# Kernel tuning notes

Measured on AMD Instinct MI355X. Metric: run time of the kernel, lower is better.

Reference implementation:

```python
import jax, jax.numpy as jnp
import numpy as np

N = 8192
D = 256

def setup_inputs() -> dict:
    key = jax.random.key(0)
    k1, k2, k3 = jax.random.split(key, 3)
    x = jax.random.normal(k1, (N, D), dtype=jnp.float32)
    adj_matrix = jax.random.uniform(k2, (N, N), dtype=jnp.float32)
    weight = jax.random.normal(k3, (D, D), dtype=jnp.float32) * 0.02
    bias = jnp.zeros((D,), dtype=jnp.float32)
    return {"x": x, "adj_matrix": adj_matrix, "weight": weight, "bias": bias}

def reference(x, adj_matrix, weight, bias):
    # degree = row sums of adjacency
    degree = jnp.sum(adj_matrix, axis=1)  # [N]
    inv_deg = 1.0 / degree               # inverse of diagonal degree matrix
    # D^-1 @ A @ D^-1 == A scaled by inv_deg on rows and columns
    normalized_adj = adj_matrix * inv_deg[:, None] * inv_deg[None, :]  # [N,N]
    h = jnp.matmul(normalized_adj, x)          # [N,D] aggregation
    h = jnp.matmul(h, weight) + bias           # [N,D] transform
    return jax.nn.relu(h)
```

## Files before the change

### kernel.cpp

```cpp
#include <hip/hip_runtime.h>
#include <stdint.h>
#include <stdio.h>

#define NROWS 8192
#define DDIM 256

typedef __attribute__((ext_vector_type(8))) __bf16 bf16x8;
typedef __attribute__((ext_vector_type(4))) float f32x4;
typedef __attribute__((address_space(3))) uint32_t as3u32;
typedef __attribute__((address_space(1))) uint32_t as1u32;

__device__ __forceinline__ void glds16(const void* g, void* l) {
  __builtin_amdgcn_global_load_lds((const as1u32*)g, (as3u32*)l, 16, 0, 0);
}

__device__ __forceinline__ ushort f2b(float f) {
  uint32_t u = __float_as_uint(f);
  return (ushort)((u + 0x7FFFu + ((u >> 16) & 1u)) >> 16);
}

__global__ __launch_bounds__(256) void degree_cast_kernel(const float* __restrict__ A,
                                                          ushort* __restrict__ Ab,
                                                          float* __restrict__ inv_deg) {
  const int row = blockIdx.x * 4 + (threadIdx.x >> 6);
  const int lane = threadIdx.x & 63;
  const float4* r4 = (const float4*)(A + (size_t)row * NROWS);
  ushort* wr = Ab + (size_t)row * NROWS;
  float s = 0.f;
#pragma unroll
  for (int i = 0; i < 32; ++i) {
    float4 v = r4[lane + (i << 6)];
    s += (v.x + v.y) + (v.z + v.w);
    ushort4 b;
    b.x = f2b(v.x); b.y = f2b(v.y); b.z = f2b(v.z); b.w = f2b(v.w);
    *(ushort4*)(wr + (size_t)(lane + (i << 6)) * 4) = b;
  }
#pragma unroll
  for (int o = 32; o > 0; o >>= 1) s += __shfl_xor(s, o, 64);
  if (lane == 0) inv_deg[row] = 1.0f / s;
}

__global__ __launch_bounds__(256) void transpose_scale_kernel(const float* __restrict__ src,
                                                              const float* __restrict__ scale,
                                                              ushort* __restrict__ dst, int K) {
  __shared__ ushort tile[64 * 256];
  const int k0 = blockIdx.x * 64;
  const int w = threadIdx.x >> 6;
  const int lane = threadIdx.x & 63;
#pragma unroll
  for (int i = 0; i < 16; ++i) {
    const int r = w * 16 + i;
    float4 v = *(const float4*)(src + (size_t)(k0 + r) * DDIM + lane * 4);
    const float sc = scale ? scale[k0 + r] : 1.0f;
    ushort4 b;
    b.x = f2b(v.x * sc); b.y = f2b(v.y * sc);
    b.z = f2b(v.z * sc); b.w = f2b(v.w * sc);
    *(ushort4*)&tile[r * 256 + lane * 4] = b;
  }
  __syncthreads();
  const int c = threadIdx.x;
  ushort* drow = dst + (size_t)c * K + k0;
#pragma unroll
  for (int s = 0; s < 8; ++s) {
    uint32_t p[4];
#pragma unroll
    for (int j = 0; j < 4; ++j) {
      uint32_t lo = tile[(s * 8 + 2 * j + 0) * 256 + c];
      uint32_t hi = tile[(s * 8 + 2 * j + 1) * 256 + c];
      p[j] = lo | (hi << 16);
    }
    uint4 u; u.x = p[0]; u.y = p[1]; u.z = p[2]; u.w = p[3];
    *(uint4*)(drow + s * 8) = u;
  }
}

__global__ __launch_bounds__(256, 2) void gemm_big_kernel(
    const ushort* __restrict__ Ab,
    const ushort* __restrict__ Bt,
    const float* __restrict__ rowscale,
    float* __restrict__ Cpart) {
  __shared__ ushort Asm[2][64 * 64];
  __shared__ ushort Bsm[2][256 * 64];

  const int tid = threadIdx.x;
  const int lane = tid & 63;
  const int w = tid >> 6;

  const int ks = blockIdx.x & 3;
  const int mb = blockIdx.x >> 2;
  const int m0 = mb * 64;
  const size_t kstart = (size_t)ks * 2048;

  const int al_r = lane >> 3;
  const int al_c = lane & 7;
  const int asw = al_c ^ al_r;
  const char* agA = (const char*)(Ab + (size_t)(m0 + 16 * w + al_r) * NROWS + kstart) + asw * 16;
  const char* bgB = (const char*)(Bt + (size_t)(64 * w + al_r) * NROWS + kstart) + asw * 16;
  const size_t grp = (size_t)8 * NROWS * 2;

  const int fr = lane & 15;
  const int q = lane >> 4;
  const int fsw = fr & 7;

  f32x4 acc[4][4] = {};
  const int NT = 2048 / 64;

  auto stage = [&](int buf, int t) {
    const size_t koff = (size_t)t * 128;
    glds16(agA + koff, &Asm[buf][(16 * w + 0) * 64]);
    glds16(agA + grp + koff, &Asm[buf][(16 * w + 8) * 64]);
#pragma unroll
    for (int j = 0; j < 8; ++j)
      glds16(bgB + (size_t)j * grp + koff, &Bsm[buf][(64 * w + 8 * j) * 64]);
  };

  stage(0, 0);
  int cur = 0;
  for (int t = 0; t < NT; ++t) {
    __syncthreads();
    if (t + 1 < NT) stage(cur ^ 1, t + 1);
#pragma unroll
    for (int kk = 0; kk < 2; ++kk) {
      uint4 af[4], bfr[4];
#pragma unroll
      for (int m = 0; m < 4; ++m)
        af[m] = *(const uint4*)((const char*)&Asm[cur][0] +
                 ((16 * m + fr) * 128 + (((4 * kk + q) ^ fsw) << 4)));
#pragma unroll
      for (int n = 0; n < 4; ++n)
        bfr[n] = *(const uint4*)((const char*)&Bsm[cur][0] +
                 ((64 * w + 16 * n + fr) * 128 + (((4 * kk + q) ^ fsw) << 4)));
#pragma unroll
      for (int m = 0; m < 4; ++m)
#pragma unroll
        for (int n = 0; n < 4; ++n)
          acc[m][n] = __builtin_amdgcn_mfma_f32_16x16x32_bf16(
              __builtin_bit_cast(bf16x8, af[m]), __builtin_bit_cast(bf16x8, bfr[n]),
              acc[m][n], 0, 0, 0);
    }
    cur ^= 1;
  }

  float* Cp = Cpart + (size_t)ks * ((size_t)NROWS * DDIM);
#pragma unroll
  for (int m = 0; m < 4; ++m)
#pragma unroll
    for (int r = 0; r < 4; ++r) {
      const int row = m0 + 16 * m + q * 4 + r;
      const float sc = rowscale[row];
#pragma unroll
      for (int n = 0; n < 4; ++n) {
        const int col = 64 * w + 16 * n + fr;
        Cp[(size_t)row * DDIM + col] = acc[m][n][r] * sc;
      }
    }
}

__global__ __launch_bounds__(512, 4) void gemm_small_kernel(
    const float* __restrict__ Hp,
    const ushort* __restrict__ Bt,
    const float* __restrict__ bias, float* __restrict__ C) {
  const int K = DDIM;
  const size_t PS = (size_t)NROWS * DDIM;
  __shared__ ushort Asm[2][32 * 32];
  __shared__ ushort Bsm[2][256 * 32];

  const int tid = threadIdx.x;
  const int lane = tid & 63;
  const int w = tid >> 6;
  const int m0 = blockIdx.x * 32;

  f32x4 acc[2][2] = {};
  const int NT = K >> 5;

  const int arow = tid >> 3;
  const int aseg = tid & 7;
  const float* ag = Hp + (size_t)(m0 + arow) * DDIM + aseg * 4;
  const int awoff = arow * 32 + ((((aseg >> 1) ^ ((arow >> 1) & 3)) << 3) | ((aseg & 1) << 2));

  const int bch0 = w * 2;
  const int bq = lane >> 2;
  const int bswz = (lane & 3) ^ ((lane >> 3) & 3);
  const char* bg0 = (const char*)Bt + (size_t)(bch0 * 16 + bq) * ((size_t)K * 2) + bswz * 16;
  const char* bg1 = bg0 + (size_t)16 * ((size_t)K * 2);

  const int fr = lane & 15;
  const int fsw = (fr >> 1) & 3;
  const int fch = (lane >> 4) ^ fsw;
  const int aoff0 = fr * 32 + (fch << 3);
  const int aoff1 = (16 + fr) * 32 + (fch << 3);
  const int boff0 = (w * 32 + fr) * 32 + (fch << 3);
  const int boff1 = (w * 32 + 16 + fr) * 32 + (fch << 3);

  auto loadA = [&](int t) {
    float4 u0 = *(const float4*)(ag + 0 * PS + t * 32);
    float4 u1 = *(const float4*)(ag + 1 * PS + t * 32);
    float4 u2 = *(const float4*)(ag + 2 * PS + t * 32);
    float4 u3 = *(const float4*)(ag + 3 * PS + t * 32);
    float4 v;
    v.x = (u0.x + u1.x) + (u2.x + u3.x);
    v.y = (u0.y + u1.y) + (u2.y + u3.y);
    v.z = (u0.z + u1.z) + (u2.z + u3.z);
    v.w = (u0.w + u1.w) + (u2.w + u3.w);
    return v;
  };

  if (tid < 256) {
    float4 v = loadA(0);
    ushort4 b; b.x = f2b(v.x); b.y = f2b(v.y); b.z = f2b(v.z); b.w = f2b(v.w);
    *(ushort4*)&Asm[0][awoff] = b;
  }
  glds16(bg0, &Bsm[0][(bch0 + 0) * 512]);
  glds16(bg1, &Bsm[0][(bch0 + 1) * 512]);

  int cur = 0;
  for (int t = 0; t < NT; ++t) {
    __syncthreads();
    const bool pf = (t + 1 < NT);
    float4 av;
    if (pf) {
      if (tid < 256) av = loadA(t + 1);
      glds16(bg0 + (size_t)(t + 1) * 64, &Bsm[cur ^ 1][(bch0 + 0) * 512]);
      glds16(bg1 + (size_t)(t + 1) * 64, &Bsm[cur ^ 1][(bch0 + 1) * 512]);
    }
    uint4 a0 = *(const uint4*)&Asm[cur][aoff0];
    uint4 a1 = *(const uint4*)&Asm[cur][aoff1];
    uint4 b0 = *(const uint4*)&Bsm[cur][boff0];
    uint4 b1 = *(const uint4*)&Bsm[cur][boff1];
    acc[0][0] = __builtin_amdgcn_mfma_f32_16x16x32_bf16(
        __builtin_bit_cast(bf16x8, a0), __builtin_bit_cast(bf16x8, b0), acc[0][0], 0, 0, 0);
    acc[0][1] = __builtin_amdgcn_mfma_f32_16x16x32_bf16(
        __builtin_bit_cast(bf16x8, a0), __builtin_bit_cast(bf16x8, b1), acc[0][1], 0, 0, 0);
    acc[1][0] = __builtin_amdgcn_mfma_f32_16x16x32_bf16(
        __builtin_bit_cast(bf16x8, a1), __builtin_bit_cast(bf16x8, b0), acc[1][0], 0, 0, 0);
    acc[1][1] = __builtin_amdgcn_mfma_f32_16x16x32_bf16(
        __builtin_bit_cast(bf16x8, a1), __builtin_bit_cast(bf16x8, b1), acc[1][1], 0, 0, 0);
    if (pf && tid < 256) {
      ushort4 b; b.x = f2b(av.x); b.y = f2b(av.y); b.z = f2b(av.z); b.w = f2b(av.w);
      *(ushort4*)&Asm[cur ^ 1][awoff] = b;
    }
    cur ^= 1;
  }

#pragma unroll
  for (int m = 0; m < 2; ++m)
#pragma unroll
    for (int n = 0; n < 2; ++n) {
      const int col = w * 32 + n * 16 + fr;
      const float bv = bias[col];
#pragma unroll
      for (int r = 0; r < 4; ++r) {
        const int row = m0 + m * 16 + (lane >> 4) * 4 + r;
        float x = acc[m][n][r] + bv;
        x = fmaxf(x, 0.f);
        C[(size_t)row * DDIM + col] = x;
      }
    }
}

extern "C" void kernel_launch(void* const* d_in, const int* in_sizes, int n_in,
                              void* d_out, int out_size, void* d_ws, size_t ws_size,
                              hipStream_t stream) {
  const float* x      = (const float*)d_in[0];
  const float* adj    = (const float*)d_in[1];
  const float* weight = (const float*)d_in[2];
  const float* bias   = (const float*)d_in[3];
  float* out = (float*)d_out;

  char* ws = (char*)d_ws;
  const size_t ab_bytes = (size_t)NROWS * NROWS * 2;
  const size_t h_bytes  = 4ull * NROWS * DDIM * 4;
  const size_t yt_bytes = (size_t)DDIM * NROWS * 2;
  const size_t wt_bytes = (size_t)DDIM * DDIM * 2;
  ushort* Ab      = (ushort*)ws;
  float*  hpart   = (float*)(ws + ab_bytes);
  ushort* Yt      = (ushort*)(ws + ab_bytes + h_bytes);
  ushort* Wt      = (ushort*)(ws + ab_bytes + h_bytes + yt_bytes);
  float*  inv_deg = (float*)(ws + ab_bytes + h_bytes + yt_bytes + wt_bytes);
  const size_t need = ab_bytes + h_bytes + yt_bytes + wt_bytes + (size_t)NROWS * 4;
  if (ws_size < need) { fprintf(stderr, "ws too small: %zu < %zu\n", ws_size, need); return; }

  degree_cast_kernel<<<NROWS / 4, 256, 0, stream>>>(adj, Ab, inv_deg);
  transpose_scale_kernel<<<NROWS / 64, 256, 0, stream>>>(x, inv_deg, Yt, NROWS);
  transpose_scale_kernel<<<DDIM / 64, 256, 0, stream>>>(weight, nullptr, Wt, DDIM);
  gemm_big_kernel<<<dim3(512), 256, 0, stream>>>(Ab, Yt, inv_deg, hpart);
  gemm_small_kernel<<<dim3(256), 512, 0, stream>>>(hpart, Wt, bias, out);
}
```

Measured before the change: 463.8 us.

## Deepen GEMM prefetch to two stages, merge transpose launches, nontemporal adjacency loads

The big GEMM now prefetches two k-tiles ahead, using explicit vmcnt waits and a split barrier. All LDS fragments are read into registers before the next global-to-LDS load is issued into the buffer just freed. The two transpose/scale launches become one launch that picks x or W by block index, saving a kernel launch. The degree/cast kernel reads the adjacency with nontemporal loads to reduce cache pollution. The hand-written waitcnt counts depend on how many loads each stage issues, so they are fragile. Holding fragments for both kk halves also raises register pressure.

```diff
diff --git a/kernel.cpp b/kernel.cpp
--- a/kernel.cpp
+++ b/kernel.cpp
@@ -24,15 +24,15 @@
                                                           float* __restrict__ inv_deg) {
   const int row = blockIdx.x * 4 + (threadIdx.x >> 6);
   const int lane = threadIdx.x & 63;
-  const float4* r4 = (const float4*)(A + (size_t)row * NROWS);
+  const f32x4* r4 = (const f32x4*)(A + (size_t)row * NROWS);
   ushort* wr = Ab + (size_t)row * NROWS;
   float s = 0.f;
 #pragma unroll
   for (int i = 0; i < 32; ++i) {
-    float4 v = r4[lane + (i << 6)];
-    s += (v.x + v.y) + (v.z + v.w);
+    f32x4 v = __builtin_nontemporal_load(r4 + lane + (i << 6));
+    s += (v[0] + v[1]) + (v[2] + v[3]);
     ushort4 b;
-    b.x = f2b(v.x); b.y = f2b(v.y); b.z = f2b(v.z); b.w = f2b(v.w);
+    b.x = f2b(v[0]); b.y = f2b(v[1]); b.z = f2b(v[2]); b.w = f2b(v[3]);
     *(ushort4*)(wr + (size_t)(lane + (i << 6)) * 4) = b;
   }
 #pragma unroll
@@ -40,11 +40,17 @@
   if (lane == 0) inv_deg[row] = 1.0f / s;
 }
 
-__global__ __launch_bounds__(256) void transpose_scale_kernel(const float* __restrict__ src,
-                                                              const float* __restrict__ scale,
-                                                              ushort* __restrict__ dst, int K) {
+__global__ __launch_bounds__(256) void transpose_scale_kernel(const float* __restrict__ x,
+                                                              const float* __restrict__ W,
+                                                              const float* __restrict__ inv_deg,
+                                                              ushort* __restrict__ Yt,
+                                                              ushort* __restrict__ Wt) {
   __shared__ ushort tile[64 * 256];
-  const int k0 = blockIdx.x * 64;
+  const int bid = blockIdx.x;
+  const float* src; ushort* dst; int K; const float* scale; int k0;
+  if (bid < 128) { src = x; dst = Yt; K = NROWS; scale = inv_deg; k0 = bid * 64; }
+  else           { src = W; dst = Wt; K = DDIM;  scale = nullptr; k0 = (bid - 128) * 64; }
+
   const int w = threadIdx.x >> 6;
   const int lane = threadIdx.x & 63;
 #pragma unroll
@@ -115,29 +121,39 @@
   };
 
   stage(0, 0);
+  stage(1, 1);
+
   int cur = 0;
   for (int t = 0; t < NT; ++t) {
-    __syncthreads();
-    if (t + 1 < NT) stage(cur ^ 1, t + 1);
+    if (t + 1 < NT) { asm volatile("s_waitcnt vmcnt(10)" ::: "memory"); }
+    else            { asm volatile("s_waitcnt vmcnt(0)" ::: "memory"); }
+    __builtin_amdgcn_s_barrier();
+
+    uint4 af[2][4], bfr[2][4];
 #pragma unroll
     for (int kk = 0; kk < 2; ++kk) {
-      uint4 af[4], bfr[4];
 #pragma unroll
       for (int m = 0; m < 4; ++m)
-        af[m] = *(const uint4*)((const char*)&Asm[cur][0] +
-                 ((16 * m + fr) * 128 + (((4 * kk + q) ^ fsw) << 4)));
+        af[kk][m] = *(const uint4*)((const char*)&Asm[cur][0] +
+                     ((16 * m + fr) * 128 + (((4 * kk + q) ^ fsw) << 4)));
 #pragma unroll
       for (int n = 0; n < 4; ++n)
-        bfr[n] = *(const uint4*)((const char*)&Bsm[cur][0] +
-                 ((64 * w + 16 * n + fr) * 128 + (((4 * kk + q) ^ fsw) << 4)));
+        bfr[kk][n] = *(const uint4*)((const char*)&Bsm[cur][0] +
+                      ((64 * w + 16 * n + fr) * 128 + (((4 * kk + q) ^ fsw) << 4)));
+    }
+    asm volatile("s_waitcnt lgkmcnt(0)" ::: "memory");
+    __builtin_amdgcn_s_barrier();
+    if (t + 2 < NT) stage(cur, t + 2);
+
+#pragma unroll
+    for (int kk = 0; kk < 2; ++kk)
 #pragma unroll
       for (int m = 0; m < 4; ++m)
 #pragma unroll
         for (int n = 0; n < 4; ++n)
           acc[m][n] = __builtin_amdgcn_mfma_f32_16x16x32_bf16(
-              __builtin_bit_cast(bf16x8, af[m]), __builtin_bit_cast(bf16x8, bfr[n]),
+              __builtin_bit_cast(bf16x8, af[kk][m]), __builtin_bit_cast(bf16x8, bfr[kk][n]),
               acc[m][n], 0, 0, 0);
-    }
     cur ^= 1;
   }
 
@@ -281,8 +297,7 @@
   if (ws_size < need) { fprintf(stderr, "ws too small: %zu < %zu\n", ws_size, need); return; }
 
   degree_cast_kernel<<<NROWS / 4, 256, 0, stream>>>(adj, Ab, inv_deg);
-  transpose_scale_kernel<<<NROWS / 64, 256, 0, stream>>>(x, inv_deg, Yt, NROWS);
-  transpose_scale_kernel<<<DDIM / 64, 256, 0, stream>>>(weight, nullptr, Wt, DDIM);
+  transpose_scale_kernel<<<128 + DDIM / 64, 256, 0, stream>>>(x, weight, inv_deg, Yt, Wt);
   gemm_big_kernel<<<dim3(512), 256, 0, stream>>>(Ab, Yt, inv_deg, hpart);
   gemm_small_kernel<<<dim3(256), 512, 0, stream>>>(hpart, Wt, bias, out);
 }
```

Result: faster. 417.9 us (-9.9%).
